# Performance work log

Hardware: AMD Instinct MI355X
Metric: run time of the kernel (lower is better)

The kernel has to match this reference:

```python
import jax, jax.numpy as jnp
import numpy as np

N = 2048        # tokens (batch*seq)
H = 4096        # hidden_size (LLaMA-7B)
I = 11008       # intermediate_size (LLaMA-7B)
QMAX = 127.0    # int8 symmetric quant range


def setup_inputs() -> dict:
    key = jax.random.key(0)
    ks = jax.random.split(key, 6)
    # pre-quantized int8 activations (stored as int32) + per-token dynamic scales
    x_q = jax.random.randint(ks[0], (N, H), -127, 128, dtype=jnp.int32)
    x_scale = jax.random.uniform(ks[1], (N,), dtype=jnp.float32) * 0.01 + 1e-4
    # fused [gate; up] int8 weight [2I, H] with per-output-channel scales
    w_gateup = jax.random.randint(ks[2], (2 * I, H), -127, 128, dtype=jnp.int32)
    w_gateup_scale = jax.random.uniform(ks[3], (2 * I,), dtype=jnp.float32) * 0.005 + 1e-4
    # down_proj int8 weight [H, I] with per-output-channel scales
    w_down = jax.random.randint(ks[4], (H, I), -127, 128, dtype=jnp.int32)
    w_down_scale = jax.random.uniform(ks[5], (H,), dtype=jnp.float32) * 0.005 + 1e-4
    return {"x_q": x_q, "x_scale": x_scale, "w_gateup": w_gateup,
            "w_gateup_scale": w_gateup_scale, "w_down": w_down,
            "w_down_scale": w_down_scale}


def reference(x_q, x_scale, w_gateup, w_gateup_scale, w_down, w_down_scale):
    acc = jnp.matmul(x_q, w_gateup.T)                      # [N, 2I] int32
    gateup = acc.astype(jnp.float32) * x_scale[:, None] * w_gateup_scale[None, :]
    # --- fused silu_and_mul + dynamic per-token requantization ---
    gate, up = jnp.split(gateup, 2, axis=-1)               # each [N, I]
    act = jax.nn.silu(gate) * up                           # [N, I]
    s2 = jnp.max(jnp.abs(act), axis=-1) / QMAX             # [N] dynamic scale
    q2 = jnp.clip(jnp.round(act / s2[:, None]), -QMAX, QMAX)  # requantized int8 (as f32)
    out = jnp.matmul(q2, w_down.T.astype(jnp.float32)) * s2[:, None] * w_down_scale[None, :]
    return out                                             # [N, H]
```

## Files before the change

kernel.cpp:

```cpp
#include <hip/hip_runtime.h>
#include <stdint.h>

typedef int i32x4 __attribute__((ext_vector_type(4)));
typedef unsigned short u16x8 __attribute__((ext_vector_type(8)));

#define N_TOK 2048
#define HID   4096
#define INTER 11008
#define TWOI  22016
#define KT1   32
#define KT2   86
#define NT1   172
#define NT2   32
#define MTI   16

#define GLD16(gp, lp) __builtin_amdgcn_global_load_lds( \
    (const __attribute__((address_space(1))) void*)(gp), \
    (__attribute__((address_space(3))) void*)(lp), 16, 0, 0)

__device__ __forceinline__ unsigned short f2bf(float f) {
  uint32_t u = __float_as_uint(f);
  uint32_t r = (u + 0x7fffu + ((u >> 16) & 1u)) >> 16;
  return (unsigned short)r;
}

__device__ __forceinline__ float bf2f(unsigned short b) {
  return __uint_as_float(((uint32_t)b) << 16);
}

__global__ __launch_bounds__(256) void pack_tiled(
    const int* __restrict__ src, uint8_t* __restrict__ dst, int K, int KT)
{
  const long u = (long)blockIdx.x * 256 + threadIdx.x;
  const long tile = u >> 10;
  const int within = (int)(u & 1023);
  const int row = within >> 3;
  const int swc = (within & 7) << 4;
  const int col = swc ^ ((row & 7) << 4);
  const long tR = tile / KT;
  const long tK = tile - tR * KT;
  const int* s = src + (tR * 128 + row) * (long)K + tK * 128 + col;
  i32x4 o;
#pragma unroll
  for (int q = 0; q < 4; ++q) {
    i32x4 w = *reinterpret_cast<const i32x4*>(s + q * 4);
    o[q] = (w[0] & 255) | ((w[1] & 255) << 8) | ((w[2] & 255) << 16)
         | ((w[3] & 255) << 24);
  }
  *reinterpret_cast<i32x4*>(dst + tile * 16384 + (long)within * 16) = o;
}

#define GEMM_PROLOGUE(AT, BT, KT)                                              \
  __shared__ uint8_t As[16384];                                                \
  __shared__ uint8_t Bs[16384];                                                \
  const int tid = threadIdx.x;                                                 \
  const int lane = tid & 63, wid = tid >> 6;                                   \
  const int mt = blockIdx.x, nt = blockIdx.y;                                  \
  const uint8_t* ga = (AT) + ((size_t)mt * (KT)) * 16384 + wid * 1024 + lane * 16; \
  const uint8_t* gb = (BT) + ((size_t)nt * (KT)) * 16384 + wid * 1024 + lane * 16; \
  uint8_t* lA = &As[wid * 1024 + lane * 16];                                   \
  uint8_t* lB = &Bs[wid * 1024 + lane * 16];                                   \
  const int r15 = lane & 15, g16 = (lane >> 4) << 4;                           \
  const int wm = (wid >> 1) << 6, wn = (wid & 1) << 6;                         \
  int rA[4], sA[4], rB[4], sB[4];                                              \
  _Pragma("unroll")                                                            \
  for (int m = 0; m < 4; ++m) {                                                \
    int ra = wm + m * 16 + r15;                                                \
    rA[m] = ra * 128; sA[m] = (ra & 7) << 4;                                   \
    int rb = wn + m * 16 + r15;                                                \
    rB[m] = rb * 128; sB[m] = (rb & 7) << 4;                                   \
  }                                                                            \
  i32x4 acc[4][4] = {};                                                        \
  for (int kt = 0; kt < (KT); ++kt) {                                          \
    _Pragma("unroll")                                                          \
    for (int i = 0; i < 4; ++i) {                                              \
      GLD16(ga + i * 4096, lA + i * 4096);                                     \
      GLD16(gb + i * 4096, lB + i * 4096);                                     \
    }                                                                          \
    ga += 16384; gb += 16384;                                                  \
    __syncthreads();                                                           \
    _Pragma("unroll")                                                          \
    for (int kk = 0; kk < 2; ++kk) {                                           \
      const int cK = g16 + kk * 64;                                            \
      i32x4 av[4], bv[4];                                                      \
      _Pragma("unroll")                                                        \
      for (int m = 0; m < 4; ++m)                                              \
        av[m] = *reinterpret_cast<const i32x4*>(&As[rA[m] + (cK ^ sA[m])]);    \
      _Pragma("unroll")                                                        \
      for (int n = 0; n < 4; ++n)                                              \
        bv[n] = *reinterpret_cast<const i32x4*>(&Bs[rB[n] + (cK ^ sB[n])]);    \
      _Pragma("unroll")                                                        \
      for (int m = 0; m < 4; ++m)                                              \
        _Pragma("unroll")                                                      \
        for (int n = 0; n < 4; ++n)                                            \
          acc[m][n] = __builtin_amdgcn_mfma_i32_16x16x64_i8(av[m], bv[n],      \
                                                            acc[m][n], 0, 0, 0); \
    }                                                                          \
    __syncthreads();                                                           \
  }                                                                            \
  const int crow0 = mt * 128 + wm + ((lane >> 4) << 2);                        \
  const int ccol0 = nt * 128 + wn + r15;

__global__ __launch_bounds__(256, 2) void gemm1_k(
    const uint8_t* __restrict__ At, const uint8_t* __restrict__ Bt,
    const float* __restrict__ xs, const float* __restrict__ wgs,
    unsigned short* __restrict__ gu)
{
  GEMM_PROLOGUE(At, Bt, KT1)
#pragma unroll
  for (int m = 0; m < 4; ++m) {
#pragma unroll
    for (int r = 0; r < 4; ++r) {
      const int row = crow0 + m * 16 + r;
      const float xr = xs[row];
      unsigned short* op = gu + (size_t)row * TWOI + ccol0;
#pragma unroll
      for (int n = 0; n < 4; ++n) {
        float v = (float)acc[m][n][r] * xr * wgs[ccol0 + n * 16];
        op[n * 16] = f2bf(v);
      }
    }
  }
}

__global__ __launch_bounds__(256, 2) void gemm2_k(
    const uint8_t* __restrict__ At, const uint8_t* __restrict__ Bt,
    const float* __restrict__ mx, const float* __restrict__ wds,
    float* __restrict__ out)
{
  GEMM_PROLOGUE(At, Bt, KT2)
#pragma unroll
  for (int m = 0; m < 4; ++m) {
#pragma unroll
    for (int r = 0; r < 4; ++r) {
      const int row = crow0 + m * 16 + r;
      const float s2 = mx[row] * (1.0f / 127.0f);
      float* op = out + (size_t)row * HID + ccol0;
#pragma unroll
      for (int n = 0; n < 4; ++n)
        op[n * 16] = (float)acc[m][n][r] * s2 * wds[ccol0 + n * 16];
    }
  }
}

__global__ __launch_bounds__(256) void rowmax_k(
    const unsigned short* __restrict__ gu, float* __restrict__ mx)
{
  const int row = blockIdx.x;
  const unsigned short* gp = gu + (size_t)row * TWOI;
  float m = 0.f;
  for (int i = threadIdx.x; i < INTER / 8; i += 256) {
    u16x8 gv = *reinterpret_cast<const u16x8*>(gp + i * 8);
    u16x8 uv = *reinterpret_cast<const u16x8*>(gp + INTER + i * 8);
#pragma unroll
    for (int j = 0; j < 8; ++j) {
      float gf = bf2f(gv[j]);
      float uf = bf2f(uv[j]);
      float a = (gf / (1.f + __expf(-gf))) * uf;
      m = fmaxf(m, __builtin_fabsf(a));
    }
  }
#pragma unroll
  for (int o = 32; o; o >>= 1) m = fmaxf(m, __shfl_xor(m, o, 64));
  __shared__ float red[4];
  const int lane = threadIdx.x & 63, wid = threadIdx.x >> 6;
  if (lane == 0) red[wid] = m;
  __syncthreads();
  if (threadIdx.x == 0)
    mx[row] = fmaxf(fmaxf(red[0], red[1]), fmaxf(red[2], red[3]));
}

__global__ __launch_bounds__(256) void quant_k(
    const unsigned short* __restrict__ gu, const float* __restrict__ mx,
    uint8_t* __restrict__ q2t)
{
  const long u = (long)blockIdx.x * 256 + threadIdx.x;
  const long tile = u >> 10;
  const int within = (int)(u & 1023);
  const int row = within >> 3;
  const int swc = (within & 7) << 4;
  const int col = swc ^ ((row & 7) << 4);
  const long tR = tile / KT2;
  const long tK = tile - tR * KT2;
  const int grow = (int)tR * 128 + row;
  const int gcol = (int)tK * 128 + col;
  const unsigned short* gp = gu + (size_t)grow * TWOI + gcol;
  const float inv = 127.0f / fmaxf(mx[grow], 1e-30f);
  u16x8 ga0 = *reinterpret_cast<const u16x8*>(gp);
  u16x8 ga1 = *reinterpret_cast<const u16x8*>(gp + 8);
  u16x8 ua0 = *reinterpret_cast<const u16x8*>(gp + INTER);
  u16x8 ua1 = *reinterpret_cast<const u16x8*>(gp + INTER + 8);
  i32x4 o;
#pragma unroll
  for (int q = 0; q < 4; ++q) {
    uint32_t d = 0;
#pragma unroll
    for (int b = 0; b < 4; ++b) {
      const int j = q * 4 + b;
      uint32_t gB = (j < 8) ? ga0[j] : ga1[j - 8];
      uint32_t uB = (j < 8) ? ua0[j] : ua1[j - 8];
      float gf = __uint_as_float(gB << 16);
      float uf = __uint_as_float(uB << 16);
      float a = (gf / (1.f + __expf(-gf))) * uf;
      float r = rintf(a * inv);
      r = fminf(fmaxf(r, -127.f), 127.f);
      d |= ((uint32_t)((int)r & 255)) << (8 * b);
    }
    o[q] = (int)d;
  }
  *reinterpret_cast<i32x4*>(q2t + tile * 16384 + (long)within * 16) = o;
}

extern "C" void kernel_launch(void* const* d_in, const int* in_sizes, int n_in,
                              void* d_out, int out_size, void* d_ws, size_t ws_size,
                              hipStream_t stream)
{
  const int*   x_q = (const int*)d_in[0];
  const float* xs  = (const float*)d_in[1];
  const int*   wg  = (const int*)d_in[2];
  const float* wgs = (const float*)d_in[3];
  const int*   wd  = (const int*)d_in[4];
  const float* wds = (const float*)d_in[5];
  float* out = (float*)d_out;

  uint8_t* ws = (uint8_t*)d_ws;
  uint8_t* x8t  = ws;
  uint8_t* wg8t = x8t + 8388608;
  uint8_t* wd8t = wg8t + 90177536;
  unsigned short* gu = (unsigned short*)(wd8t + 45088768);
  float* mx = (float*)((uint8_t*)gu + 90177536);
  uint8_t* q2t = (uint8_t*)mx + 8192;

  pack_tiled<<<2048, 256, 0, stream>>>(x_q, x8t, HID, KT1);
  pack_tiled<<<22016, 256, 0, stream>>>(wg, wg8t, HID, KT1);
  pack_tiled<<<11008, 256, 0, stream>>>(wd, wd8t, INTER, KT2);

  gemm1_k<<<dim3(MTI, NT1), 256, 0, stream>>>(x8t, wg8t, xs, wgs, gu);
  rowmax_k<<<N_TOK, 256, 0, stream>>>(gu, mx);
  quant_k<<<5504, 256, 0, stream>>>(gu, mx, q2t);
  gemm2_k<<<dim3(MTI, NT2), 256, 0, stream>>>(q2t, wd8t, mx, wds, out);
}
```

Measured before the change: 461.2 us.

## Fuse SiLU-mul and row-max into gemm1 epilogue with larger double-buffered tiles

Gemm1 now uses 512-thread blocks covering 256 rows by matching 128-column gate and up tiles. SiLU*up is applied in the epilogue through LDS, only the bf16 activation is written, and the per-row absmax is accumulated with atomicMax. This removes the rowmax kernel and halves the intermediate tensor traffic. Both GEMMs gain double-buffered LDS prefetch, s_setprio around the MFMAs, and larger tiles (gemm2 now 128x256). The cost is much larger LDS use (128KB in gemm1), which limits occupancy, plus atomics and an extra zeroing launch.

```diff
diff --git a/kernel.cpp b/kernel.cpp
--- a/kernel.cpp
+++ b/kernel.cpp
@@ -10,9 +10,6 @@
 #define TWOI  22016
 #define KT1   32
 #define KT2   86
-#define NT1   172
-#define NT2   32
-#define MTI   16
 
 #define GLD16(gp, lp) __builtin_amdgcn_global_load_lds( \
     (const __attribute__((address_space(1))) void*)(gp), \
@@ -22,10 +19,6 @@
   uint32_t u = __float_as_uint(f);
   uint32_t r = (u + 0x7fffu + ((u >> 16) & 1u)) >> 16;
   return (unsigned short)r;
-}
-
-__device__ __forceinline__ float bf2f(unsigned short b) {
-  return __uint_as_float(((uint32_t)b) << 16);
 }
 
 __global__ __launch_bounds__(256) void pack_tiled(
@@ -50,128 +43,138 @@
   *reinterpret_cast<i32x4*>(dst + tile * 16384 + (long)within * 16) = o;
 }
 
-#define GEMM_PROLOGUE(AT, BT, KT)                                              \
-  __shared__ uint8_t As[16384];                                                \
-  __shared__ uint8_t Bs[16384];                                                \
-  const int tid = threadIdx.x;                                                 \
-  const int lane = tid & 63, wid = tid >> 6;                                   \
-  const int mt = blockIdx.x, nt = blockIdx.y;                                  \
-  const uint8_t* ga = (AT) + ((size_t)mt * (KT)) * 16384 + wid * 1024 + lane * 16; \
-  const uint8_t* gb = (BT) + ((size_t)nt * (KT)) * 16384 + wid * 1024 + lane * 16; \
-  uint8_t* lA = &As[wid * 1024 + lane * 16];                                   \
-  uint8_t* lB = &Bs[wid * 1024 + lane * 16];                                   \
-  const int r15 = lane & 15, g16 = (lane >> 4) << 4;                           \
-  const int wm = (wid >> 1) << 6, wn = (wid & 1) << 6;                         \
-  int rA[4], sA[4], rB[4], sB[4];                                              \
-  _Pragma("unroll")                                                            \
-  for (int m = 0; m < 4; ++m) {                                                \
-    int ra = wm + m * 16 + r15;                                                \
-    rA[m] = ra * 128; sA[m] = (ra & 7) << 4;                                   \
-    int rb = wn + m * 16 + r15;                                                \
-    rB[m] = rb * 128; sB[m] = (rb & 7) << 4;                                   \
-  }                                                                            \
-  i32x4 acc[4][4] = {};                                                        \
-  for (int kt = 0; kt < (KT); ++kt) {                                          \
-    _Pragma("unroll")                                                          \
-    for (int i = 0; i < 4; ++i) {                                              \
-      GLD16(ga + i * 4096, lA + i * 4096);                                     \
-      GLD16(gb + i * 4096, lB + i * 4096);                                     \
-    }                                                                          \
-    ga += 16384; gb += 16384;                                                  \
-    __syncthreads();                                                           \
-    _Pragma("unroll")                                                          \
-    for (int kk = 0; kk < 2; ++kk) {                                           \
-      const int cK = g16 + kk * 64;                                            \
-      i32x4 av[4], bv[4];                                                      \
-      _Pragma("unroll")                                                        \
-      for (int m = 0; m < 4; ++m)                                              \
-        av[m] = *reinterpret_cast<const i32x4*>(&As[rA[m] + (cK ^ sA[m])]);    \
-      _Pragma("unroll")                                                        \
-      for (int n = 0; n < 4; ++n)                                              \
-        bv[n] = *reinterpret_cast<const i32x4*>(&Bs[rB[n] + (cK ^ sB[n])]);    \
-      _Pragma("unroll")                                                        \
-      for (int m = 0; m < 4; ++m)                                              \
-        _Pragma("unroll")                                                      \
-        for (int n = 0; n < 4; ++n)                                            \
-          acc[m][n] = __builtin_amdgcn_mfma_i32_16x16x64_i8(av[m], bv[n],      \
-                                                            acc[m][n], 0, 0, 0); \
-    }                                                                          \
-    __syncthreads();                                                           \
-  }                                                                            \
-  const int crow0 = mt * 128 + wm + ((lane >> 4) << 2);                        \
-  const int ccol0 = nt * 128 + wn + r15;
-
-__global__ __launch_bounds__(256, 2) void gemm1_k(
-    const uint8_t* __restrict__ At, const uint8_t* __restrict__ Bt,
+__global__ __launch_bounds__(1024) void zero_mx(float* __restrict__ mx) {
+  const int i = blockIdx.x * 1024 + threadIdx.x;
+  if (i < N_TOK) mx[i] = 0.0f;
+}
+
+__global__ __launch_bounds__(512, 2) void gemm1_k(
+    const uint8_t* __restrict__ x8t, const uint8_t* __restrict__ wg8t,
     const float* __restrict__ xs, const float* __restrict__ wgs,
-    unsigned short* __restrict__ gu)
-{
-  GEMM_PROLOGUE(At, Bt, KT1)
-#pragma unroll
-  for (int m = 0; m < 4; ++m) {
-#pragma unroll
-    for (int r = 0; r < 4; ++r) {
-      const int row = crow0 + m * 16 + r;
-      const float xr = xs[row];
-      unsigned short* op = gu + (size_t)row * TWOI + ccol0;
+    unsigned short* __restrict__ act, float* __restrict__ mx)
+{
+  __shared__ uint8_t sm[131072];
+  const int tid = threadIdx.x;
+  const int lane = tid & 63, wid = tid >> 6;
+  const int wgm = wid >> 2, wgn = wid & 3;
+  const int mt = blockIdx.x, nt = blockIdx.y;
+  const int r15 = lane & 15;
+  const int sxo = (r15 & 7) << 4;
+  const int khi = (lane >> 4) << 4;
+
+  const uint8_t* pA0 = x8t  + ((size_t)(2 * mt)     * KT1) * 16384 + tid * 16;
+  const uint8_t* pA1 = x8t  + ((size_t)(2 * mt + 1) * KT1) * 16384 + tid * 16;
+  const uint8_t* pB0 = wg8t + ((size_t)nt           * KT1) * 16384 + tid * 16;
+  const uint8_t* pB1 = wg8t + ((size_t)(86 + nt)    * KT1) * 16384 + tid * 16;
+
+  const int aoff = ((wgm << 7) + r15) << 7;
+  const int boff = 32768 + (((wgn << 6) + r15) << 7);
+
+  i32x4 acc[8][4] = {};
+
+#define STAGE1(kt, buf) do {                                   \
+    uint8_t* l = sm + (buf) * 65536;                           \
+    const size_t S = (size_t)(kt) * 16384;                     \
+    GLD16(pA0 + S,        l + tid * 16);                       \
+    GLD16(pA0 + S + 8192, l + tid * 16 + 8192);                \
+    GLD16(pA1 + S,        l + tid * 16 + 16384);               \
+    GLD16(pA1 + S + 8192, l + tid * 16 + 24576);               \
+    GLD16(pB0 + S,        l + tid * 16 + 32768);               \
+    GLD16(pB0 + S + 8192, l + tid * 16 + 40960);               \
+    GLD16(pB1 + S,        l + tid * 16 + 49152);               \
+    GLD16(pB1 + S + 8192, l + tid * 16 + 57344);               \
+  } while (0)
+
+  STAGE1(0, 0);
+  __syncthreads();
+
+  for (int kt = 0; kt < KT1; ++kt) {
+    if (kt + 1 < KT1) STAGE1(kt + 1, (kt + 1) & 1);
+    const uint8_t* bufc = sm + (kt & 1) * 65536;
+#pragma unroll
+    for (int kk = 0; kk < 2; ++kk) {
+      const int cs = (khi + kk * 64) ^ sxo;
+      i32x4 bv[4];
+#pragma unroll
+      for (int n = 0; n < 4; ++n)
+        bv[n] = *reinterpret_cast<const i32x4*>(bufc + boff + n * 2048 + cs);
+#pragma unroll
+      for (int mh = 0; mh < 2; ++mh) {
+        i32x4 av[4];
+#pragma unroll
+        for (int m = 0; m < 4; ++m)
+          av[m] = *reinterpret_cast<const i32x4*>(
+              bufc + aoff + (mh * 4 + m) * 2048 + cs);
+        __builtin_amdgcn_s_setprio(1);
+#pragma unroll
+        for (int m = 0; m < 4; ++m)
+#pragma unroll
+          for (int n = 0; n < 4; ++n)
+            acc[mh * 4 + m][n] = __builtin_amdgcn_mfma_i32_16x16x64_i8(
+                av[m], bv[n], acc[mh * 4 + m][n], 0, 0, 0);
+        __builtin_amdgcn_s_setprio(0);
+      }
+    }
+    __syncthreads();
+  }
+#undef STAGE1
+
+  float* gs = (float*)sm;
+  const int rq = (lane >> 4) << 2;
+  if (wgn < 2) {
+#pragma unroll
+    for (int m = 0; m < 8; ++m) {
 #pragma unroll
       for (int n = 0; n < 4; ++n) {
-        float v = (float)acc[m][n][r] * xr * wgs[ccol0 + n * 16];
-        op[n * 16] = f2bf(v);
-      }
-    }
-  }
-}
-
-__global__ __launch_bounds__(256, 2) void gemm2_k(
-    const uint8_t* __restrict__ At, const uint8_t* __restrict__ Bt,
-    const float* __restrict__ mx, const float* __restrict__ wds,
-    float* __restrict__ out)
-{
-  GEMM_PROLOGUE(At, Bt, KT2)
-#pragma unroll
-  for (int m = 0; m < 4; ++m) {
-#pragma unroll
-    for (int r = 0; r < 4; ++r) {
-      const int row = crow0 + m * 16 + r;
-      const float s2 = mx[row] * (1.0f / 127.0f);
-      float* op = out + (size_t)row * HID + ccol0;
-#pragma unroll
-      for (int n = 0; n < 4; ++n)
-        op[n * 16] = (float)acc[m][n][r] * s2 * wds[ccol0 + n * 16];
-    }
-  }
-}
-
-__global__ __launch_bounds__(256) void rowmax_k(
-    const unsigned short* __restrict__ gu, float* __restrict__ mx)
-{
-  const int row = blockIdx.x;
-  const unsigned short* gp = gu + (size_t)row * TWOI;
-  float m = 0.f;
-  for (int i = threadIdx.x; i < INTER / 8; i += 256) {
-    u16x8 gv = *reinterpret_cast<const u16x8*>(gp + i * 8);
-    u16x8 uv = *reinterpret_cast<const u16x8*>(gp + INTER + i * 8);
-#pragma unroll
-    for (int j = 0; j < 8; ++j) {
-      float gf = bf2f(gv[j]);
-      float uf = bf2f(uv[j]);
-      float a = (gf / (1.f + __expf(-gf))) * uf;
-      m = fmaxf(m, __builtin_fabsf(a));
-    }
-  }
-#pragma unroll
-  for (int o = 32; o; o >>= 1) m = fmaxf(m, __shfl_xor(m, o, 64));
-  __shared__ float red[4];
-  const int lane = threadIdx.x & 63, wid = threadIdx.x >> 6;
-  if (lane == 0) red[wid] = m;
+        const int coll = (wgn << 6) + n * 16 + r15;
+        const float wsc = wgs[nt * 128 + coll];
+#pragma unroll
+        for (int r = 0; r < 4; ++r) {
+          const int rowl = (wgm << 7) + m * 16 + rq + r;
+          const float g = (float)acc[m][n][r] * xs[mt * 256 + rowl] * wsc;
+          gs[rowl * 128 + (coll ^ (((rowl >> 2) & 1) << 4))] = g;
+        }
+      }
+    }
+  }
   __syncthreads();
-  if (threadIdx.x == 0)
-    mx[row] = fmaxf(fmaxf(red[0], red[1]), fmaxf(red[2], red[3]));
+  if (wgn >= 2) {
+#pragma unroll
+    for (int m = 0; m < 8; ++m) {
+      float am[4] = {0.f, 0.f, 0.f, 0.f};
+#pragma unroll
+      for (int n = 0; n < 4; ++n) {
+        const int cu = ((wgn - 2) << 6) + n * 16 + r15;
+        const float wsc = wgs[INTER + nt * 128 + cu];
+#pragma unroll
+        for (int r = 0; r < 4; ++r) {
+          const int rowl = (wgm << 7) + m * 16 + rq + r;
+          const int grow = mt * 256 + rowl;
+          const float uv = (float)acc[m][n][r] * xs[grow] * wsc;
+          const float g = gs[rowl * 128 + (cu ^ (((rowl >> 2) & 1) << 4))];
+          const float a = g / (1.f + __expf(-g)) * uv;
+          act[(size_t)grow * INTER + nt * 128 + cu] = f2bf(a);
+          am[r] = fmaxf(am[r], __builtin_fabsf(a));
+        }
+      }
+#pragma unroll
+      for (int r = 0; r < 4; ++r) {
+#pragma unroll
+        for (int off = 1; off < 16; off <<= 1)
+          am[r] = fmaxf(am[r], __shfl_xor(am[r], off, 64));
+      }
+      if (r15 == 0) {
+#pragma unroll
+        for (int r = 0; r < 4; ++r)
+          atomicMax((int*)&mx[mt * 256 + (wgm << 7) + m * 16 + rq + r],
+                    __float_as_int(am[r]));
+      }
+    }
+  }
 }
 
 __global__ __launch_bounds__(256) void quant_k(
-    const unsigned short* __restrict__ gu, const float* __restrict__ mx,
+    const unsigned short* __restrict__ act, const float* __restrict__ mx,
     uint8_t* __restrict__ q2t)
 {
   const long u = (long)blockIdx.x * 256 + threadIdx.x;
@@ -184,12 +187,10 @@
   const long tK = tile - tR * KT2;
   const int grow = (int)tR * 128 + row;
   const int gcol = (int)tK * 128 + col;
-  const unsigned short* gp = gu + (size_t)grow * TWOI + gcol;
+  const unsigned short* ap = act + (size_t)grow * INTER + gcol;
   const float inv = 127.0f / fmaxf(mx[grow], 1e-30f);
-  u16x8 ga0 = *reinterpret_cast<const u16x8*>(gp);
-  u16x8 ga1 = *reinterpret_cast<const u16x8*>(gp + 8);
-  u16x8 ua0 = *reinterpret_cast<const u16x8*>(gp + INTER);
-  u16x8 ua1 = *reinterpret_cast<const u16x8*>(gp + INTER + 8);
+  u16x8 a0 = *reinterpret_cast<const u16x8*>(ap);
+  u16x8 a1 = *reinterpret_cast<const u16x8*>(ap + 8);
   i32x4 o;
 #pragma unroll
   for (int q = 0; q < 4; ++q) {
@@ -197,18 +198,95 @@
 #pragma unroll
     for (int b = 0; b < 4; ++b) {
       const int j = q * 4 + b;
-      uint32_t gB = (j < 8) ? ga0[j] : ga1[j - 8];
-      uint32_t uB = (j < 8) ? ua0[j] : ua1[j - 8];
-      float gf = __uint_as_float(gB << 16);
-      float uf = __uint_as_float(uB << 16);
-      float a = (gf / (1.f + __expf(-gf))) * uf;
-      float r = rintf(a * inv);
+      uint32_t aB = (j < 8) ? a0[j] : a1[j - 8];
+      float af = __uint_as_float(aB << 16);
+      float r = rintf(af * inv);
       r = fminf(fmaxf(r, -127.f), 127.f);
       d |= ((uint32_t)((int)r & 255)) << (8 * b);
     }
     o[q] = (int)d;
   }
   *reinterpret_cast<i32x4*>(q2t + tile * 16384 + (long)within * 16) = o;
+}
+
+__global__ __launch_bounds__(512, 2) void gemm2_k(
+    const uint8_t* __restrict__ q2t, const uint8_t* __restrict__ wd8t,
+    const float* __restrict__ mx, const float* __restrict__ wds,
+    float* __restrict__ out)
+{
+  __shared__ uint8_t sm[98304];
+  const int tid = threadIdx.x;
+  const int lane = tid & 63, wid = tid >> 6;
+  const int wgm = wid >> 2, wgn = wid & 3;
+  const int mt = blockIdx.x, nt = blockIdx.y;
+  const int r15 = lane & 15;
+  const int sxo = (r15 & 7) << 4;
+  const int khi = (lane >> 4) << 4;
+
+  const uint8_t* pA  = q2t  + ((size_t)mt           * KT2) * 16384 + tid * 16;
+  const uint8_t* pB0 = wd8t + ((size_t)(2 * nt)     * KT2) * 16384 + tid * 16;
+  const uint8_t* pB1 = wd8t + ((size_t)(2 * nt + 1) * KT2) * 16384 + tid * 16;
+
+  const int aoff = ((wgm << 6) + r15) << 7;
+  const int boff = 16384 + (((wgn << 6) + r15) << 7);
+
+  i32x4 acc[4][4] = {};
+
+#define STAGE2(kt, buf) do {                                   \
+    uint8_t* l = sm + (buf) * 49152;                           \
+    const size_t S = (size_t)(kt) * 16384;                     \
+    GLD16(pA  + S,        l + tid * 16);                       \
+    GLD16(pA  + S + 8192, l + tid * 16 + 8192);                \
+    GLD16(pB0 + S,        l + tid * 16 + 16384);               \
+    GLD16(pB0 + S + 8192, l + tid * 16 + 24576);               \
+    GLD16(pB1 + S,        l + tid * 16 + 32768);               \
+    GLD16(pB1 + S + 8192, l + tid * 16 + 40960);               \
+  } while (0)
+
+  STAGE2(0, 0);
+  __syncthreads();
+
+  for (int kt = 0; kt < KT2; ++kt) {
+    if (kt + 1 < KT2) STAGE2(kt + 1, (kt + 1) & 1);
+    const uint8_t* bufc = sm + (kt & 1) * 49152;
+#pragma unroll
+    for (int kk = 0; kk < 2; ++kk) {
+      const int cs = (khi + kk * 64) ^ sxo;
+      i32x4 av[4], bv[4];
+#pragma unroll
+      for (int n = 0; n < 4; ++n)
+        bv[n] = *reinterpret_cast<const i32x4*>(bufc + boff + n * 2048 + cs);
+#pragma unroll
+      for (int m = 0; m < 4; ++m)
+        av[m] = *reinterpret_cast<const i32x4*>(bufc + aoff + m * 2048 + cs);
+      __builtin_amdgcn_s_setprio(1);
+#pragma unroll
+      for (int m = 0; m < 4; ++m)
+#pragma unroll
+        for (int n = 0; n < 4; ++n)
+          acc[m][n] = __builtin_amdgcn_mfma_i32_16x16x64_i8(
+              av[m], bv[n], acc[m][n], 0, 0, 0);
+      __builtin_amdgcn_s_setprio(0);
+    }
+    __syncthreads();
+  }
+#undef STAGE2
+
+  const int rq = (lane >> 4) << 2;
+#pragma unroll
+  for (int m = 0; m < 4; ++m) {
+#pragma unroll
+    for (int r = 0; r < 4; ++r) {
+      const int rowl = (wgm << 6) + m * 16 + rq + r;
+      const int grow = mt * 128 + rowl;
+      const float s2 = mx[grow] * (1.0f / 127.0f);
+      float* op = out + (size_t)grow * HID + nt * 256 + (wgn << 6) + r15;
+      const float* wp = wds + nt * 256 + (wgn << 6) + r15;
+#pragma unroll
+      for (int n = 0; n < 4; ++n)
+        op[n * 16] = (float)acc[m][n][r] * s2 * wp[n * 16];
+    }
+  }
 }
 
 extern "C" void kernel_launch(void* const* d_in, const int* in_sizes, int n_in,
@@ -227,16 +305,16 @@
   uint8_t* x8t  = ws;
   uint8_t* wg8t = x8t + 8388608;
   uint8_t* wd8t = wg8t + 90177536;
-  unsigned short* gu = (unsigned short*)(wd8t + 45088768);
-  float* mx = (float*)((uint8_t*)gu + 90177536);
+  unsigned short* act = (unsigned short*)(wd8t + 45088768);
+  float* mx = (float*)((uint8_t*)act + 45088768);
   uint8_t* q2t = (uint8_t*)mx + 8192;
 
+  zero_mx<<<2, 1024, 0, stream>>>(mx);
   pack_tiled<<<2048, 256, 0, stream>>>(x_q, x8t, HID, KT1);
   pack_tiled<<<22016, 256, 0, stream>>>(wg, wg8t, HID, KT1);
   pack_tiled<<<11008, 256, 0, stream>>>(wd, wd8t, INTER, KT2);
 
-  gemm1_k<<<dim3(MTI, NT1), 256, 0, stream>>>(x8t, wg8t, xs, wgs, gu);
-  rowmax_k<<<N_TOK, 256, 0, stream>>>(gu, mx);
-  quant_k<<<5504, 256, 0, stream>>>(gu, mx, q2t);
-  gemm2_k<<<dim3(MTI, NT2), 256, 0, stream>>>(q2t, wd8t, mx, wds, out);
-}
+  gemm1_k<<<dim3(8, 86), 512, 0, stream>>>(x8t, wg8t, xs, wgs, act, mx);
+  quant_k<<<5504, 256, 0, stream>>>(act, mx, q2t);
+  gemm2_k<<<dim3(16, 16), 512, 0, stream>>>(q2t, wd8t, mx, wds, out);
+}
```

New measurement: 461.5 us. About the same (+0.1%).
